# Performance work log

Measured on AMD Instinct MI355X. Metric: run time of the kernel, lower is better.

## Reference

```python
import jax, jax.numpy as jnp
import numpy as np

V = 32000; D = 1024; L = 2; H = 16; KVH = 4; HD = D // H; E = 8; FF = 2048; K = 2
B = 2; S = 1024; WINDOW = 4096; THETA = 10000.0; EPS = 1e-6


def setup_inputs() -> dict:
    key = jax.random.key(0)
    ks = jax.random.split(key, 12)
    std = 0.02
    return {
        'tokens': jax.random.randint(ks[0], (B, S), 0, V),
        'tok_emb': jax.random.normal(ks[1], (V, D), jnp.float32),  # nn.Embedding default N(0,1)
        'norm1_w': jnp.ones((L, D), jnp.float32),
        'norm2_w': jnp.ones((L, D), jnp.float32),
        'wq': jax.random.normal(ks[2], (L, D, D), jnp.float32) * std,
        'wk': jax.random.normal(ks[3], (L, KVH * HD, D), jnp.float32) * std,
        'wv': jax.random.normal(ks[4], (L, KVH * HD, D), jnp.float32) * std,
        'wo': jax.random.normal(ks[5], (L, D, D), jnp.float32) * std,
        'router_w': jax.random.normal(ks[6], (L, E, D), jnp.float32) * (std / np.sqrt(D)),
        'w1': jax.random.normal(ks[7], (L, E, FF, D), jnp.float32) * std,
        'w2': jax.random.normal(ks[8], (L, E, FF, D), jnp.float32) * std,
        'w3': jax.random.normal(ks[9], (L, E, D, FF), jnp.float32) * std,
        'normf_w': jnp.ones((D,), jnp.float32),
        'head_w': jax.random.normal(ks[10], (V, D), jnp.float32) * std,
    }


def rmsnorm(x, w):
    # F.normalize(x, dim=-1, eps) * w * sqrt(d)
    n = jnp.linalg.norm(x, axis=-1, keepdims=True)
    return x / jnp.maximum(n, EPS) * w * np.float32(np.sqrt(x.shape[-1]))


def rope(x, cos, sin):
    # x: (b, s, h, hd); pairs are interleaved (even, odd) per view_as_complex
    x2 = x.reshape(x.shape[:-1] + (-1, 2))
    x0, x1 = x2[..., 0], x2[..., 1]
    o0 = x0 * cos - x1 * sin
    o1 = x0 * sin + x1 * cos
    return jnp.stack([o0, o1], axis=-1).reshape(x.shape)


def attention(x, wq, wk, wv, wo, cos, sin):
    b, s, _ = x.shape
    q = (x @ wq.T).reshape(b, s, H, HD)
    k = (x @ wk.T).reshape(b, s, KVH, HD)
    v = (x @ wv.T).reshape(b, s, KVH, HD)
    q = rope(q, cos, sin)
    k = rope(k, cos, sin)
    g = H // KVH
    k = jnp.repeat(k, g, axis=2)
    v = jnp.repeat(v, g, axis=2)
    scores = jnp.einsum('bqhd,bkhd->bhqk', q, k) / np.float32(np.sqrt(HD))
    i = jnp.arange(s)[:, None]; j = jnp.arange(s)[None, :]
    allow = (j <= i) & (i - j < WINDOW)  # causal + sliding window
    scores = jnp.where(allow, scores, -jnp.inf)
    attn = jax.nn.softmax(scores, axis=-1)
    out = jnp.einsum('bhqk,bkhd->bqhd', attn, v).reshape(b, s, D)
    return out @ wo.T


def moe(x, router_w, w1, w2, w3):
    b, s, d = x.shape
    logits = jnp.einsum('bsd,ed->bse', x, router_w)
    probs = jax.nn.softmax(logits, axis=-1)
    _, idx = jax.lax.top_k(probs, K)                      # (b, s, K)
    mask = jax.nn.one_hot(idx, E, dtype=x.dtype).sum(-2)  # (b, s, E) binary
    xt = x.reshape(-1, d)           # (T, d)
    mt = mask.reshape(-1, E)        # (T, E)
    # Dense masked dispatch: every expert computed on all tokens, combine masks to zero
    u = jnp.einsum('td,efd->etf', xt, w1)
    g = jax.nn.silu(u) * jnp.einsum('td,efd->etf', xt, w2)
    y = jnp.einsum('etf,edf->etd', g, w3)
    out = jnp.einsum('etd,te->td', y, mt).reshape(b, s, d)  # unweighted combine (per source)
    # aux losses
    z_loss = jnp.mean(jax.scipy.special.logsumexp(logits, axis=-1)) ** 2
    load = probs.sum(axis=0)  # (s, E), matching probs.sum(dim=0) in source
    load_loss = (jnp.std(load, ddof=1) / jnp.mean(load)) ** 2
    aux = 0.001 * z_loss + 0.001 * load_loss
    return out, aux


def _rope_tables(dtype):
    freqs = 1.0 / (THETA ** (np.arange(0, HD, 2, dtype=np.float32) / HD))
    ang = np.arange(S, dtype=np.float32)[:, None] * freqs[None, :]
    cos = jnp.asarray(np.cos(ang), dtype)[None, :, None, :]
    sin = jnp.asarray(np.sin(ang), dtype)[None, :, None, :]
    return cos, sin


def reference(tokens, tok_emb, norm1_w, norm2_w, wq, wk, wv, wo, router_w, w1, w2, w3, normf_w, head_w):
    x = tok_emb[tokens]  # (B, S, D)
    cos, sin = _rope_tables(x.dtype)
    attn_scale = np.float32(1.0 / np.sqrt(2.0 * L))
    aux_total = jnp.zeros((), x.dtype)
    for l in range(L):
        x = x + attn_scale * attention(rmsnorm(x, norm1_w[l]), wq[l], wk[l], wv[l], wo[l], cos, sin)
        mo, aux = moe(rmsnorm(x, norm2_w[l]), router_w[l], w1[l], w2[l], w3[l])
        x = x + mo
        aux_total = aux_total + aux
    logits = rmsnorm(x, normf_w) @ head_w.T
    return logits, aux_total
```

## Files before the change

kernel.cpp:

```cpp
#include <hip/hip_runtime.h>
#include <math.h>

#define DEV __device__ __forceinline__

using v8s = __attribute__((ext_vector_type(8))) short;
using v4f = __attribute__((ext_vector_type(4))) float;

DEV short f2bf(float f) {
    unsigned u = __float_as_uint(f);
    unsigned r = (u + 0x7fffu + ((u >> 16) & 1u)) >> 16;
    return (short)(unsigned short)r;
}
DEV float bf2f(short s) {
    return __uint_as_float(((unsigned)(unsigned short)s) << 16);
}

DEV void gload16(const short* g, short* l) {
    __builtin_amdgcn_global_load_lds((const __attribute__((address_space(1))) void*)g,
                                     (__attribute__((address_space(3))) void*)l,
                                     16, 0, 0);
}

DEV void raw_barrier() { asm volatile("s_barrier" ::: "memory"); }

DEV float block_sum256(float v, float* red) {
    __syncthreads();
#pragma unroll
    for (int o = 32; o >= 1; o >>= 1) v += __shfl_down(v, o, 64);
    if ((threadIdx.x & 63) == 0) red[threadIdx.x >> 6] = v;
    __syncthreads();
    return red[0] + red[1] + red[2] + red[3];
}
DEV float block_max256(float v, float* red) {
    __syncthreads();
#pragma unroll
    for (int o = 32; o >= 1; o >>= 1) v = fmaxf(v, __shfl_down(v, o, 64));
    if ((threadIdx.x & 63) == 0) red[threadIdx.x >> 6] = v;
    __syncthreads();
    return fmaxf(fmaxf(red[0], red[1]), fmaxf(red[2], red[3]));
}


__global__ __launch_bounds__(256) void conv_tile(const float* __restrict__ src,
                                                 short* __restrict__ hi, short* __restrict__ lo,
                                                 long nGroups, int Kg, long chunkRows, long chunkPanelStride) {
    const long panelElems = 128L * Kg * 8;
    for (long idx = (long)blockIdx.x * 256 + threadIdx.x; idx < nGroups; idx += (long)gridDim.x * 256) {
        long rrow = idx / Kg; int g = (int)(idx - rrow * Kg);
        long c = rrow / chunkRows; int ri = (int)(rrow - c * chunkRows);
        long panel = c * chunkPanelStride + (ri >> 7);
        long dst = panel * panelElems + ((long)(g >> 2) << 12) + ((long)(g & 3) << 10) + ((long)(ri & 127) << 3);
        const float4 f0 = ((const float4*)src)[idx * 2];
        const float4 f1 = ((const float4*)src)[idx * 2 + 1];
        short h0 = f2bf(f0.x), h1 = f2bf(f0.y), h2 = f2bf(f0.z), h3 = f2bf(f0.w);
        short h4 = f2bf(f1.x), h5 = f2bf(f1.y), h6 = f2bf(f1.z), h7 = f2bf(f1.w);
        *(ushort4*)(hi + dst)     = make_ushort4((unsigned short)h0, (unsigned short)h1,
                                                 (unsigned short)h2, (unsigned short)h3);
        *(ushort4*)(hi + dst + 4) = make_ushort4((unsigned short)h4, (unsigned short)h5,
                                                 (unsigned short)h6, (unsigned short)h7);
        if (lo) {
            short l0 = f2bf(f0.x - bf2f(h0)), l1 = f2bf(f0.y - bf2f(h1));
            short l2 = f2bf(f0.z - bf2f(h2)), l3 = f2bf(f0.w - bf2f(h3));
            short l4 = f2bf(f1.x - bf2f(h4)), l5 = f2bf(f1.y - bf2f(h5));
            short l6 = f2bf(f1.z - bf2f(h6)), l7 = f2bf(f1.w - bf2f(h7));
            *(ushort4*)(lo + dst)     = make_ushort4((unsigned short)l0, (unsigned short)l1,
                                                     (unsigned short)l2, (unsigned short)l3);
            *(ushort4*)(lo + dst + 4) = make_ushort4((unsigned short)l4, (unsigned short)l5,
                                                     (unsigned short)l6, (unsigned short)l7);
        }
    }
}

struct GemmP {
    const short* Ah; const short* Al;
    const short* Bh; const short* Bl;
    float* C; short* Ch; short* Cl;
    const int* cnt; const int* ppd; const int* lrow;
    long aPanelsZ;
    long strideAz;
    long strideBz, strideCz;
    int M, N, K, lda, ldc;
    float alpha;
    int outMode;
    int gqaB;
    int grouped;
    int causalSkip;
    int ntiles, G, Gx;
};

template<bool SPLIT>
__global__ __launch_bounds__(256) void gemm_bt128(GemmP p) {
    const int lid = blockIdx.x;
    const int xcd = lid & 7, sI = lid >> 3;
    const int gx = sI % p.Gx;
    const int mt = sI / p.Gx;
    const int gi = xcd + 8 * gx;
    if (gi >= p.G) return;
    const int nt = gi % p.ntiles;
    const int z  = gi / p.ntiles;
    if (p.causalSkip && nt > mt) return;

    const int tid = threadIdx.x;
    int Mz = p.grouped ? p.cnt[z] : p.M;
    if (mt * 128 >= Mz) return;

    long bOff;
    if (p.gqaB) { int b = z >> 4, h = z & 15; bOff = (long)(b * 4 + (h >> 2)) * p.strideBz; }
    else bOff = (long)z * p.strideBz;

    extern __shared__ short s0[];
    const int BUF = SPLIT ? 16384 : 8192;

    const int lane = tid & 63, w = tid >> 6;
    const int lr = lane & 15, lg = lane >> 4;
    const int wr = w >> 1, wc = w & 1;

    v4f acc[4][4];
#pragma unroll
    for (int i = 0; i < 4; ++i)
#pragma unroll
        for (int j = 0; j < 4; ++j) { acc[i][j][0] = 0.f; acc[i][j][1] = 0.f; acc[i][j][2] = 0.f; acc[i][j][3] = 0.f; }

    const short* bks  = p.Bh + bOff + (long)nt * 128 * p.K + (long)w * 1024 + lane * 8;
    const short* bksL = SPLIT ? p.Bl + bOff + (long)nt * 128 * p.K + (long)w * 1024 + lane * 8 : nullptr;

    long aPanel = (p.grouped ? (long)(p.ppd[z] >> 7) : (long)z * p.aPanelsZ) + mt;
    const short* aks  = p.Ah + aPanel * 128L * p.K + (long)w * 1024 + lane * 8;
    const short* aksL = SPLIT ? p.Al + aPanel * 128L * p.K + (long)w * 1024 + lane * 8 : nullptr;

    const int nIter = p.K >> 5;
    const int wb = w * 1024;
    {
        gload16(aks,       s0 + wb);
        gload16(aks + 512, s0 + wb + 512);
        gload16(bks,       s0 + 4096 + wb);
        gload16(bks + 512, s0 + 4096 + wb + 512);
        if (SPLIT) {
            gload16(aksL,       s0 + 8192 + wb);
            gload16(aksL + 512, s0 + 8192 + wb + 512);
            gload16(bksL,       s0 + 12288 + wb);
            gload16(bksL + 512, s0 + 12288 + wb + 512);
        }
    }
    for (int i = 0; i < nIter; ++i) {
        const int cur = i & 1;
        if (i + 1 < nIter) {
            raw_barrier();
            const long kb = (long)(i + 1) * 4096;
            short* base = s0 + (cur ^ 1) * BUF;
            gload16(aks + kb,       base + wb);
            gload16(aks + kb + 512, base + wb + 512);
            gload16(bks + kb,       base + 4096 + wb);
            gload16(bks + kb + 512, base + 4096 + wb + 512);
            if (SPLIT) {
                gload16(aksL + kb,       base + 8192 + wb);
                gload16(aksL + kb + 512, base + 8192 + wb + 512);
                gload16(bksL + kb,       base + 12288 + wb);
                gload16(bksL + kb + 512, base + 12288 + wb + 512);
            }
            if constexpr (SPLIT) asm volatile("s_waitcnt vmcnt(8)" ::: "memory");
            else                 asm volatile("s_waitcnt vmcnt(4)" ::: "memory");
        } else {
            asm volatile("s_waitcnt vmcnt(0)" ::: "memory");
        }
        raw_barrier();
        const short* base = s0 + cur * BUF;
        const int abase = lg * 1024 + (wr * 64 + lr) * 8;
        const int bbase = 4096 + lg * 1024 + (wc * 64 + lr) * 8;
        v8s ah[4], bh[4];
#pragma unroll
        for (int q = 0; q < 4; ++q) {
            ah[q] = *(const v8s*)(base + abase + q * 128);
            bh[q] = *(const v8s*)(base + bbase + q * 128);
        }
        if constexpr (SPLIT) {
            v8s al[4], bl[4];
#pragma unroll
            for (int q = 0; q < 4; ++q) {
                al[q] = *(const v8s*)(base + 8192 + abase + q * 128);
                bl[q] = *(const v8s*)(base + 8192 + bbase + q * 128);
            }
#pragma unroll
            for (int mi = 0; mi < 4; ++mi)
#pragma unroll
                for (int nj = 0; nj < 4; ++nj) {
                    acc[mi][nj] = __builtin_amdgcn_mfma_f32_16x16x32_bf16(ah[mi], bh[nj], acc[mi][nj], 0, 0, 0);
                    acc[mi][nj] = __builtin_amdgcn_mfma_f32_16x16x32_bf16(al[mi], bh[nj], acc[mi][nj], 0, 0, 0);
                    acc[mi][nj] = __builtin_amdgcn_mfma_f32_16x16x32_bf16(ah[mi], bl[nj], acc[mi][nj], 0, 0, 0);
                }
        } else {
#pragma unroll
            for (int mi = 0; mi < 4; ++mi)
#pragma unroll
                for (int nj = 0; nj < 4; ++nj)
                    acc[mi][nj] = __builtin_amdgcn_mfma_f32_16x16x32_bf16(ah[mi], bh[nj], acc[mi][nj], 0, 0, 0);
        }
    }

#pragma unroll
    for (int mi = 0; mi < 4; ++mi) {
        const int mrow = mt * 128 + wr * 64 + mi * 16 + lg * 4;
#pragma unroll
        for (int nj = 0; nj < 4; ++nj) {
            const int ncol = nt * 128 + wc * 64 + nj * 16 + lr;
            if (ncol < p.N) {
#pragma unroll
                for (int rr = 0; rr < 4; ++rr) {
                    const int m = mrow + rr;
                    if (m < Mz) {
                        float v = acc[mi][nj][rr] * p.alpha;
                        long crow;
                        if (p.grouped == 1)      crow = p.ppd[z] + m;
                        else if (p.grouped == 2) crow = p.lrow[z * 2048 + m];
                        else                     crow = m;
                        long co = (long)z * p.strideCz + crow * (long)p.ldc + ncol;
                        if (p.outMode == 0) p.C[co] = v;
                        else                p.C[co] += v;
                    }
                }
            }
        }
    }
}

template<bool SPLIT>
__global__ __launch_bounds__(512) void gemm_bt256(GemmP p) {
    const int lid = blockIdx.x;
    const int xcd = lid & 7, sI = lid >> 3;
    const int gx = sI % p.Gx;
    const int mt = sI / p.Gx;
    const int gi = xcd + 8 * gx;
    if (gi >= p.G) return;
    const int nt = gi % p.ntiles;
    const int z  = gi / p.ntiles;
    if (p.causalSkip && nt > 2 * mt + 1) return;

    const int tid = threadIdx.x;
    int Mz = p.grouped ? p.cnt[z] : p.M;
    if (mt * 256 >= Mz) return;

    long bOff;
    if (p.gqaB) { int b = z >> 4, h = z & 15; bOff = (long)(b * 4 + (h >> 2)) * p.strideBz; }
    else bOff = (long)z * p.strideBz;

    extern __shared__ short s0[];
    const int BUF = SPLIT ? 24576 : 12288;

    const int lane = tid & 63, w = tid >> 6;
    const int lr = lane & 15, lg = lane >> 4;
    const int wr = w >> 1, wc = w & 1;

    v4f acc[4][4];
#pragma unroll
    for (int i = 0; i < 4; ++i)
#pragma unroll
        for (int j = 0; j < 4; ++j) { acc[i][j][0] = 0.f; acc[i][j][1] = 0.f; acc[i][j][2] = 0.f; acc[i][j][3] = 0.f; }

    const short* bks  = p.Bh + bOff + (long)nt * 128 * p.K + (long)w * 512 + lane * 8;
    const short* bksL = SPLIT ? p.Bl + bOff + (long)nt * 128 * p.K + (long)w * 512 + lane * 8 : nullptr;
    const long aPanelBase = (p.grouped ? (long)(p.ppd[z] >> 7) : (long)z * p.aPanelsZ) + 2L * mt;
    const int u0 = 2 * w, u1 = 2 * w + 1;
    const short* aks0  = p.Ah + (aPanelBase + (u0 >> 3)) * 128L * p.K + (long)(u0 & 7) * 512 + lane * 8;
    const short* aks1  = p.Ah + (aPanelBase + (u1 >> 3)) * 128L * p.K + (long)(u1 & 7) * 512 + lane * 8;
    const short* aks0L = SPLIT ? p.Al + (aPanelBase + (u0 >> 3)) * 128L * p.K + (long)(u0 & 7) * 512 + lane * 8 : nullptr;
    const short* aks1L = SPLIT ? p.Al + (aPanelBase + (u1 >> 3)) * 128L * p.K + (long)(u1 & 7) * 512 + lane * 8 : nullptr;
    short* dA0 = s0 + u0 * 512;
    short* dA1 = s0 + u1 * 512;
    short* dB  = s0 + 8192 + w * 512;

    const int nIter = p.K >> 5;
    {
        gload16(aks0, dA0);
        gload16(aks1, dA1);
        gload16(bks,  dB);
        if (SPLIT) {
            gload16(aks0L, dA0 + 12288);
            gload16(aks1L, dA1 + 12288);
            gload16(bksL,  dB + 12288);
        }
    }
    for (int i = 0; i < nIter; ++i) {
        const int cur = i & 1;
        if (i + 1 < nIter) {
            raw_barrier();
            const long kb = (long)(i + 1) * 4096;
            const int boff = (cur ^ 1) * BUF;
            gload16(aks0 + kb, dA0 + boff);
            gload16(aks1 + kb, dA1 + boff);
            gload16(bks + kb,  dB + boff);
            if (SPLIT) {
                gload16(aks0L + kb, dA0 + boff + 12288);
                gload16(aks1L + kb, dA1 + boff + 12288);
                gload16(bksL + kb,  dB + boff + 12288);
            }
            if constexpr (SPLIT) asm volatile("s_waitcnt vmcnt(6)" ::: "memory");
            else                 asm volatile("s_waitcnt vmcnt(3)" ::: "memory");
        } else {
            asm volatile("s_waitcnt vmcnt(0)" ::: "memory");
        }
        raw_barrier();
        const short* base = s0 + cur * BUF;
        const int abase = (wr >> 1) * 4096 + lg * 1024 + ((wr & 1) * 64 + lr) * 8;
        const int bbase = 8192 + lg * 1024 + (wc * 64 + lr) * 8;
        v8s ah[4], bh[4];
#pragma unroll
        for (int q = 0; q < 4; ++q) {
            ah[q] = *(const v8s*)(base + abase + q * 128);
            bh[q] = *(const v8s*)(base + bbase + q * 128);
        }
        if constexpr (SPLIT) {
            v8s al[4], bl[4];
#pragma unroll
            for (int q = 0; q < 4; ++q) {
                al[q] = *(const v8s*)(base + 12288 + abase + q * 128);
                bl[q] = *(const v8s*)(base + 12288 + bbase + q * 128);
            }
#pragma unroll
            for (int mi = 0; mi < 4; ++mi)
#pragma unroll
                for (int nj = 0; nj < 4; ++nj) {
                    acc[mi][nj] = __builtin_amdgcn_mfma_f32_16x16x32_bf16(ah[mi], bh[nj], acc[mi][nj], 0, 0, 0);
                    acc[mi][nj] = __builtin_amdgcn_mfma_f32_16x16x32_bf16(al[mi], bh[nj], acc[mi][nj], 0, 0, 0);
                    acc[mi][nj] = __builtin_amdgcn_mfma_f32_16x16x32_bf16(ah[mi], bl[nj], acc[mi][nj], 0, 0, 0);
                }
        } else {
#pragma unroll
            for (int mi = 0; mi < 4; ++mi)
#pragma unroll
                for (int nj = 0; nj < 4; ++nj)
                    acc[mi][nj] = __builtin_amdgcn_mfma_f32_16x16x32_bf16(ah[mi], bh[nj], acc[mi][nj], 0, 0, 0);
        }
    }

#pragma unroll
    for (int mi = 0; mi < 4; ++mi) {
        const int mrow = mt * 256 + wr * 64 + mi * 16 + lg * 4;
#pragma unroll
        for (int nj = 0; nj < 4; ++nj) {
            const int ncol = nt * 128 + wc * 64 + nj * 16 + lr;
            if (ncol < p.N) {
#pragma unroll
                for (int rr = 0; rr < 4; ++rr) {
                    const int m = mrow + rr;
                    if (m < Mz) {
                        float v = acc[mi][nj][rr] * p.alpha;
                        long crow;
                        if (p.grouped == 1)      crow = p.ppd[z] + m;
                        else if (p.grouped == 2) crow = p.lrow[z * 2048 + m];
                        else                     crow = m;
                        long co = (long)z * p.strideCz + crow * (long)p.ldc + ncol;
                        if (p.outMode == 0) p.C[co] = v;
                        else                p.C[co] += v;
                    }
                }
            }
        }
    }
}

__global__ __launch_bounds__(256) void gemm_pv(GemmP p) {
    const int lid = blockIdx.x;
    const int xcd = lid & 7, sI = lid >> 3;
    const int gx = sI % 4;
    const int mt = sI / 4;
    const int z = xcd + 8 * gx;
    const int tid = threadIdx.x;

    const int b = z >> 4, h = z & 15;
    const long bOff = (long)(b * 4 + (h >> 2)) * p.strideBz;

    extern __shared__ short s0[];
    short* Ahs = s0;
    short* Bhs = s0 + 4096;
    short* Als = s0 + 8192;
    short* Bls = s0 + 12288;

    const int lane = tid & 63, w = tid >> 6;
    const int lr = lane & 15, lg = lane >> 4;
    const int wr = w >> 1, wc = w & 1;

    v4f acc[4][4];
#pragma unroll
    for (int i = 0; i < 4; ++i)
#pragma unroll
        for (int j = 0; j < 4; ++j) { acc[i][j][0] = 0.f; acc[i][j][1] = 0.f; acc[i][j][2] = 0.f; acc[i][j][3] = 0.f; }

    const short* bks  = p.Bh + bOff + (long)w * 1024 + lane * 8;
    const short* bksL = p.Bl + bOff + (long)w * 1024 + lane * 8;

    const int r = tid & 127;
    const int kgA = tid >> 7;
    const int am = mt * 128 + r;
    const long arowoff = (long)z * p.strideAz + (long)am * p.lda;
    const short* aH = p.Ah + arowoff + kgA * 16;
    const short* aL = p.Al + arowoff + kgA * 16;
    short* sA0 = s0 + (kgA * 256 + r) * 8; short* sA1 = sA0 + 1024;
    short* sA0l = s0 + 8192 + (kgA * 256 + r) * 8; short* sA1l = sA0l + 1024;

    const int kEnd = min(p.K, (mt + 1) * 128);
    const int wb = w * 1024;
    for (int k0 = 0; k0 < kEnd; k0 += 32) {
        const long kb = (long)k0 * 128;
        uint4 a0 = *(const uint4*)(aH + k0);
        uint4 a1 = *(const uint4*)(aH + k0 + 8);
        uint4 a0l = *(const uint4*)(aL + k0);
        uint4 a1l = *(const uint4*)(aL + k0 + 8);
        __syncthreads();
        gload16(bks + kb,       Bhs + wb);
        gload16(bks + kb + 512, Bhs + wb + 512);
        gload16(bksL + kb,       Bls + wb);
        gload16(bksL + kb + 512, Bls + wb + 512);
        *(uint4*)sA0 = a0; *(uint4*)sA1 = a1;
        *(uint4*)sA0l = a0l; *(uint4*)sA1l = a1l;
        __syncthreads();
        const int abase = lg * 1024 + (wr * 64 + lr) * 8;
        const int bbase = lg * 1024 + (wc * 64 + lr) * 8;
        v8s ah[4], bh[4], al[4], bl[4];
#pragma unroll
        for (int q = 0; q < 4; ++q) {
            ah[q] = *(const v8s*)(Ahs + abase + q * 128);
            bh[q] = *(const v8s*)(Bhs + bbase + q * 128);
            al[q] = *(const v8s*)(Als + abase + q * 128);
            bl[q] = *(const v8s*)(Bls + bbase + q * 128);
        }
#pragma unroll
        for (int mi = 0; mi < 4; ++mi)
#pragma unroll
            for (int nj = 0; nj < 4; ++nj) {
                acc[mi][nj] = __builtin_amdgcn_mfma_f32_16x16x32_bf16(ah[mi], bh[nj], acc[mi][nj], 0, 0, 0);
                acc[mi][nj] = __builtin_amdgcn_mfma_f32_16x16x32_bf16(al[mi], bh[nj], acc[mi][nj], 0, 0, 0);
                acc[mi][nj] = __builtin_amdgcn_mfma_f32_16x16x32_bf16(ah[mi], bl[nj], acc[mi][nj], 0, 0, 0);
            }
    }

#pragma unroll
    for (int mi = 0; mi < 4; ++mi) {
        const int mrow = mt * 128 + wr * 64 + mi * 16 + lg * 4;
#pragma unroll
        for (int nj = 0; nj < 4; ++nj) {
            const int ncol = wc * 64 + nj * 16 + lr;
            if (ncol < 64) {
#pragma unroll
                for (int rr = 0; rr < 4; ++rr) {
                    const int m = mrow + rr;
                    float v = acc[mi][nj][rr];
                    int grow = b * 1024 + m, col = h * 64 + ncol;
                    long dst = ((long)(grow >> 7)) * 131072 + ((long)(col >> 5) << 12)
                             + ((long)((col >> 3) & 3) << 10) + ((long)(grow & 127) << 3) + (col & 7);
                    short hi = f2bf(v);
                    p.Ch[dst] = hi;
                    p.Cl[dst] = f2bf(v - bf2f(hi));
                }
            }
        }
    }
}

__global__ __launch_bounds__(256) void embed_kernel(const int* toks, const float* emb, float* X) {
    const int t = blockIdx.x;
    const int tok = toks[t];
    const float4* s = (const float4*)(emb + (size_t)tok * 1024);
    float4* d = (float4*)(X + (size_t)t * 1024);
    d[threadIdx.x] = s[threadIdx.x];
}

__global__ __launch_bounds__(256) void rmsnorm_split(const float* X, const float* w, short* oh, short* ol) {
    __shared__ float red[4];
    const long t = blockIdx.x;
    const float* r = X + t * 1024;
    float ss = 0.f;
    for (int j = threadIdx.x; j < 1024; j += 256) { float f = r[j]; ss += f * f; }
    ss = block_sum256(ss, red);
    const float sc = 32.f / fmaxf(sqrtf(ss), 1e-6f);
    if (threadIdx.x < 128) {
        const int g = threadIdx.x, f = g * 8;
        float v[8];
#pragma unroll
        for (int j = 0; j < 8; ++j) v[j] = r[f + j] * sc * w[f + j];
        long dst = (t >> 7) * 131072 + ((long)(g >> 2) << 12) + ((long)(g & 3) << 10) + ((t & 127) << 3);
        short h[8], lo[8];
#pragma unroll
        for (int j = 0; j < 8; ++j) { h[j] = f2bf(v[j]); lo[j] = f2bf(v[j] - bf2f(h[j])); }
        *(ushort4*)(oh + dst)     = make_ushort4((unsigned short)h[0], (unsigned short)h[1], (unsigned short)h[2], (unsigned short)h[3]);
        *(ushort4*)(oh + dst + 4) = make_ushort4((unsigned short)h[4], (unsigned short)h[5], (unsigned short)h[6], (unsigned short)h[7]);
        *(ushort4*)(ol + dst)     = make_ushort4((unsigned short)lo[0], (unsigned short)lo[1], (unsigned short)lo[2], (unsigned short)lo[3]);
        *(ushort4*)(ol + dst + 4) = make_ushort4((unsigned short)lo[4], (unsigned short)lo[5], (unsigned short)lo[6], (unsigned short)lo[7]);
    }
}

struct RopeF { float f[32]; };

__global__ __launch_bounds__(256) void rope_fused_kernel(const float* QKV,
                                                         short* QH, short* QL,
                                                         short* KH, short* KL,
                                                         short* VH, short* VL, RopeF rf) {
    const int bid = blockIdx.x;
    if (bid < 4096) {
        const int idx = bid * 256 + threadIdx.x;
        const int pp = idx & 31, h = (idx >> 5) & 15, s = (idx >> 9) & 1023, b = idx >> 19;
        const float* src = QKV + ((size_t)(b * 1024 + s)) * 1536 + h * 64 + 2 * pp;
        const float x0 = src[0], x1 = src[1];
        const float ang = (float)s * rf.f[pp];
        float sn, cs; sincosf(ang, &sn, &cs);
        const float o0 = x0 * cs - x1 * sn, o1 = x0 * sn + x1 * cs;
        const int z = b * 16 + h, d = 2 * pp;
        const long off = (long)z * 65536 + (long)(s >> 7) * 8192
                       + ((long)(d >> 5) << 12) + ((long)((d >> 3) & 3) << 10)
                       + ((long)(s & 127) << 3) + (d & 7);
        short h0 = f2bf(o0); QH[off] = h0; QL[off] = f2bf(o0 - bf2f(h0));
        short h1 = f2bf(o1); QH[off + 1] = h1; QL[off + 1] = f2bf(o1 - bf2f(h1));
    } else if (bid < 5120) {
        const int idx = (bid - 4096) * 256 + threadIdx.x;
        const int pp = idx & 31, kv = (idx >> 5) & 3, s = (idx >> 7) & 1023, b = idx >> 17;
        const float* src = QKV + ((size_t)(b * 1024 + s)) * 1536 + 1024 + kv * 64 + 2 * pp;
        const float x0 = src[0], x1 = src[1];
        const float ang = (float)s * rf.f[pp];
        float sn, cs; sincosf(ang, &sn, &cs);
        const float o0 = x0 * cs - x1 * sn, o1 = x0 * sn + x1 * cs;
        const int z = b * 4 + kv, d = 2 * pp;
        const long off = (long)z * 65536 + (long)(s >> 7) * 8192
                       + ((long)(d >> 5) << 12) + ((long)((d >> 3) & 3) << 10)
                       + ((long)(s & 127) << 3) + (d & 7);
        short h0 = f2bf(o0); KH[off] = h0; KL[off] = f2bf(o0 - bf2f(h0));
        short h1 = f2bf(o1); KH[off + 1] = h1; KL[off + 1] = f2bf(o1 - bf2f(h1));
    } else {
        const int idx = (bid - 5120) * 256 + threadIdx.x;
        const int d = idx & 63, kv = (idx >> 6) & 3, s = (idx >> 8) & 1023, b = idx >> 18;
        const float f = QKV[((size_t)(b * 1024 + s)) * 1536 + 1280 + kv * 64 + d];
        const int z = b * 4 + kv;
        const long off = (long)z * 131072 + ((long)(s >> 5) << 12) + ((long)((s >> 3) & 3) << 10)
                       + ((long)d << 3) + (s & 7);
        short hi = f2bf(f);
        VH[off] = hi; VL[off] = f2bf(f - bf2f(hi));
        VH[off + 512] = 0; VL[off + 512] = 0;
    }
}

__global__ __launch_bounds__(256) void attn_softmax(float* SC) {
    const long row = blockIdx.x;
    const int i = (int)(row & 1023);
    float* r = SC + row * 1024;
    __shared__ float buf[1024];
    __shared__ float red[4];
    const int n = i + 1;
    for (int j = threadIdx.x; j < n; j += 256) buf[j] = r[j];
    __syncthreads();
    float m = -INFINITY;
    for (int j = threadIdx.x; j < n; j += 256) m = fmaxf(m, buf[j]);
    m = block_max256(m, red);
    float s = 0.f;
    for (int j = threadIdx.x; j < n; j += 256) { float e = expf(buf[j] - m); buf[j] = e; s += e; }
    s = block_sum256(s, red);
    const float inv = 1.f / s;
    short* rh = (short*)r;
    short* rl = rh + 1024;
    __syncthreads();
    for (int j = threadIdx.x; j < 1024; j += 256) {
        float pv = (j < n) ? buf[j] * inv : 0.f;
        short hi = f2bf(pv);
        rh[j] = hi;
        rl[j] = f2bf(pv - bf2f(hi));
    }
}

__global__ __launch_bounds__(256) void router_kernel(const float* X, const float* wn, const float* rw,
                                                     float* probs, float* lse, int* cnt, int* ltok, int* lrow) {
    __shared__ float xs[1024];
    __shared__ float red[4];
    __shared__ float lg[8];
    const int t = blockIdx.x;
    const float* r = X + (size_t)t * 1024;
    for (int j = threadIdx.x; j < 1024; j += 256) xs[j] = r[j];
    __syncthreads();
    float ss = 0.f;
    for (int j = threadIdx.x; j < 1024; j += 256) ss += xs[j] * xs[j];
    ss = block_sum256(ss, red);
    const float sc = 32.f / fmaxf(sqrtf(ss), 1e-6f);
    float acc[8] = {0, 0, 0, 0, 0, 0, 0, 0};
    for (int j = threadIdx.x; j < 1024; j += 256) {
        const float xv = xs[j] * wn[j];
#pragma unroll
        for (int e = 0; e < 8; ++e) acc[e] += xv * rw[e * 1024 + j];
    }
#pragma unroll
    for (int e = 0; e < 8; ++e) {
        float s = block_sum256(acc[e], red);
        if (threadIdx.x == 0) lg[e] = s * sc;
    }
    __syncthreads();
    if (threadIdx.x == 0) {
        float m = lg[0];
        for (int e = 1; e < 8; ++e) m = fmaxf(m, lg[e]);
        float ex[8], se = 0.f;
        for (int e = 0; e < 8; ++e) { ex[e] = expf(lg[e] - m); se += ex[e]; }
        const float inv = 1.f / se;
        float pr[8];
        for (int e = 0; e < 8; ++e) { pr[e] = ex[e] * inv; probs[(size_t)t * 8 + e] = pr[e]; }
        lse[t] = m + logf(se);
        int i1 = 0;
        for (int e = 1; e < 8; ++e) if (pr[e] > pr[i1]) i1 = e;
        int i2 = (i1 == 0) ? 1 : 0;
        for (int e = 0; e < 8; ++e) if (e != i1 && pr[e] > pr[i2]) i2 = e;
        int s1 = atomicAdd(&cnt[i1], 1); ltok[i1 * 2048 + s1] = t; lrow[i1 * 2048 + s1] = 2 * t;
        int s2 = atomicAdd(&cnt[i2], 1); ltok[i2 * 2048 + s2] = t; lrow[i2 * 2048 + s2] = 2 * t + 1;
    }
}

__global__ void prefix_kernel(const int* cnt, int* ppd) {
    if (threadIdx.x == 0 && blockIdx.x == 0) {
        int a = 0;
        for (int e = 0; e < 8; ++e) { ppd[e] = a; a += ((cnt[e] + 255) >> 8) << 8; }
    }
}

__global__ __launch_bounds__(256) void gather_kernel(const short* XNH, const short* XNL,
                                                     const int* cnt, const int* ppd, const int* ltok,
                                                     short* GXNH, short* GXNL) {
    const int e = blockIdx.y, i = blockIdx.x;
    if (i >= cnt[e]) return;
    const int t = ltok[e * 2048 + i];
    const int pd = ppd[e] + i;
    const int plane = threadIdx.x >> 7, g = threadIdx.x & 127;
    const long goff = ((long)(g >> 2) << 12) + ((long)(g & 3) << 10);
    const long src = (long)(t >> 7) * 131072 + goff + ((t & 127) << 3);
    const long dst = (long)(pd >> 7) * 131072 + goff + ((pd & 127) << 3);
    const short* S = plane ? XNL : XNH;
    short* D = plane ? GXNL : GXNH;
    *(uint4*)(D + dst) = *(const uint4*)(S + src);
}

__global__ __launch_bounds__(256) void silu_mul(const float* U, short* HH, short* HL) {
    const int row = blockIdx.x, g = threadIdx.x;
    const float* ur = U + (long)row * 4096 + g * 8;
    const float4 u0 = *(const float4*)ur, u1 = *(const float4*)(ur + 4);
    const float4 g0 = *(const float4*)(ur + 2048), g1 = *(const float4*)(ur + 2052);
    float h[8];
    h[0] = (u0.x / (1.f + expf(-u0.x))) * g0.x;
    h[1] = (u0.y / (1.f + expf(-u0.y))) * g0.y;
    h[2] = (u0.z / (1.f + expf(-u0.z))) * g0.z;
    h[3] = (u0.w / (1.f + expf(-u0.w))) * g0.w;
    h[4] = (u1.x / (1.f + expf(-u1.x))) * g1.x;
    h[5] = (u1.y / (1.f + expf(-u1.y))) * g1.y;
    h[6] = (u1.z / (1.f + expf(-u1.z))) * g1.z;
    h[7] = (u1.w / (1.f + expf(-u1.w))) * g1.w;
    const long dst = (long)(row >> 7) * 262144 + ((long)(g >> 2) << 12) + ((long)(g & 3) << 10) + ((row & 127) << 3);
    short hh[8], ll[8];
#pragma unroll
    for (int j = 0; j < 8; ++j) { hh[j] = f2bf(h[j]); ll[j] = f2bf(h[j] - bf2f(hh[j])); }
    *(ushort4*)(HH + dst)     = make_ushort4((unsigned short)hh[0], (unsigned short)hh[1], (unsigned short)hh[2], (unsigned short)hh[3]);
    *(ushort4*)(HH + dst + 4) = make_ushort4((unsigned short)hh[4], (unsigned short)hh[5], (unsigned short)hh[6], (unsigned short)hh[7]);
    *(ushort4*)(HL + dst)     = make_ushort4((unsigned short)ll[0], (unsigned short)ll[1], (unsigned short)ll[2], (unsigned short)ll[3]);
    *(ushort4*)(HL + dst + 4) = make_ushort4((unsigned short)ll[4], (unsigned short)ll[5], (unsigned short)ll[6], (unsigned short)ll[7]);
}

__global__ __launch_bounds__(256) void combine_kernel(float* X, const float* Y) {
    const int i4 = blockIdx.x * 256 + threadIdx.x;
    const int t = i4 >> 8, d4 = i4 & 255;
    float4 x = ((float4*)X)[i4];
    const float4 a = ((const float4*)Y)[(size_t)(2 * t) * 256 + d4];
    const float4 b = ((const float4*)Y)[(size_t)(2 * t + 1) * 256 + d4];
    x.x += a.x + b.x; x.y += a.y + b.y; x.z += a.z + b.z; x.w += a.w + b.w;
    ((float4*)X)[i4] = x;
}

__global__ __launch_bounds__(256) void aux_kernel(const float* probs, const float* lse, float* auxb, int layer) {
    __shared__ float red[4];
    float sl = 0.f;
    for (int t = threadIdx.x; t < 2048; t += 256) sl += lse[t];
    sl = block_sum256(sl, red);
    float s1 = 0.f, s2 = 0.f;
    for (int i = threadIdx.x; i < 8192; i += 256) {
        const float l = probs[i] + probs[8192 + i];
        s1 += l; s2 += l * l;
    }
    s1 = block_sum256(s1, red);
    s2 = block_sum256(s2, red);
    if (threadIdx.x == 0) {
        const float ml = sl / 2048.f;
        const float mean = s1 / 8192.f;
        const float var = fmaxf((s2 - s1 * s1 / 8192.f) / 8191.f, 0.f);
        auxb[layer] = 0.001f * (ml * ml + var / (mean * mean));
    }
}

__global__ void finalize_aux(const float* auxb, float* out) {
    if (threadIdx.x == 0 && blockIdx.x == 0)
        out[(size_t)2 * 1024 * 32000] = auxb[0] + auxb[1];
}

static void run_gemm128(hipStream_t s, bool split, GemmP& p, int ntiles, int mtiles, int zdim) {
    p.ntiles = ntiles;
    p.G = ntiles * zdim;
    p.Gx = (p.G + 7) >> 3;
    long nb = 8L * p.Gx * mtiles;
    dim3 g((unsigned)nb, 1, 1), b(256);
    if (split) gemm_bt128<true><<<g, b, 65536, s>>>(p);
    else       gemm_bt128<false><<<g, b, 32768, s>>>(p);
}

static void run_gemm256(hipStream_t s, bool split, GemmP& p, int ntiles, int mtiles, int zdim) {
    p.ntiles = ntiles;
    p.G = ntiles * zdim;
    p.Gx = (p.G + 7) >> 3;
    long nb = 8L * p.Gx * mtiles;
    dim3 g((unsigned)nb, 1, 1), b(512);
    if (split) gemm_bt256<true><<<g, b, 98304, s>>>(p);
    else       gemm_bt256<false><<<g, b, 49152, s>>>(p);
}

static void run_tile(hipStream_t s, const float* src, short* hi, short* lo,
                     long rows, int K, long chunkRows, long chunkPanelStride) {
    long groups = rows * (K / 8);
    long nb = (groups + 255) / 256; if (nb > 2048) nb = 2048;
    conv_tile<<<(unsigned)nb, 256, 0, s>>>(src, hi, lo, groups, K / 8, chunkRows, chunkPanelStride);
}

extern "C" void kernel_launch(void* const* d_in, const int* in_sizes, int n_in,
                              void* d_out, int out_size, void* d_ws, size_t ws_size,
                              hipStream_t stream) {
    (void)in_sizes; (void)n_in; (void)out_size; (void)ws_size;
    const int*   tokens = (const int*)d_in[0];
    const float* tok_emb = (const float*)d_in[1];
    const float* norm1 = (const float*)d_in[2];
    const float* norm2 = (const float*)d_in[3];
    const float* wq = (const float*)d_in[4];
    const float* wk = (const float*)d_in[5];
    const float* wv = (const float*)d_in[6];
    const float* wo = (const float*)d_in[7];
    const float* rw = (const float*)d_in[8];
    const float* w1 = (const float*)d_in[9];
    const float* w2 = (const float*)d_in[10];
    const float* w3 = (const float*)d_in[11];
    const float* normf = (const float*)d_in[12];
    const float* headw = (const float*)d_in[13];
    float* out = (float*)d_out;

    char* w = (char*)d_ws;
    const size_t MB = 1024ull * 1024ull;
    float* X    = (float*)(w + 0);
    short* XNH  = (short*)(w + 8 * MB);
    short* XNL  = (short*)(w + 12 * MB);
    short* QRH  = (short*)(w + 16 * MB);
    short* QRL  = (short*)(w + 20 * MB);
    short* AOH  = QRH;
    short* AOL  = QRL;
    short* KRH  = (short*)(w + 24 * MB);
    short* KRL  = (short*)(w + 25 * MB);
    short* VTH  = (short*)(w + 26 * MB);
    short* VTL  = (short*)(w + 28 * MB);
    float* QKV  = (float*)(w + 32 * MB);
    float* SC   = (float*)(w + 32 * MB);
    short* GXNH = (short*)(w + 32 * MB);
    short* GXNL = (short*)(w + 44 * MB);
    float* U    = (float*)(w + 56 * MB);
    short* HH   = (short*)(w + 152 * MB);
    short* HL   = (short*)(w + 176 * MB);
    float* Y    = (float*)(w + 200 * MB);
    float* PROBS= (float*)(w + 216 * MB);
    float* LSE  = (float*)(w + 216 * MB + 65536);
    int*   CNT  = (int*)  (w + 216 * MB + 73728);
    int*   PPD  = (int*)  (w + 216 * MB + 73856);
    int*   LTOK = (int*)  (w + 216 * MB + 74240);
    int*   LROW = (int*)  (w + 216 * MB + 74240 + 65536);
    float* AUXB = (float*)(w + 216 * MB + 74240 + 131072);
    short* WQKVH = (short*)(w + 218 * MB);
    short* WQKVL = (short*)(w + 224 * MB);
    short* WOH   = (short*)(w + 230 * MB);
    short* WOL   = (short*)(w + 234 * MB);
    short* W12H  = (short*)(w + 238 * MB);
    short* W12L  = (short*)(w + 302 * MB);
    short* W3H   = (short*)(w + 366 * MB);
    short* W3L   = (short*)(w + 398 * MB);
    short* HDH   = (short*)(w + 302 * MB);

    RopeF rf;
    for (int i = 0; i < 32; ++i) {
        float t = (float)pow(10000.0, (double)(2 * i) / 64.0);
        rf.f[i] = 1.0f / t;
    }

    for (int l = 0; l < 2; ++l) {
        long qo = (long)l * 1572864;
        run_tile(stream, wq + (long)l * 1048576, WQKVH + qo,           WQKVL + qo,           1024, 1024, 1024, 8);
        run_tile(stream, wk + (long)l * 262144,  WQKVH + qo + 1048576, WQKVL + qo + 1048576, 256, 1024, 256, 2);
        run_tile(stream, wv + (long)l * 262144,  WQKVH + qo + 1310720, WQKVL + qo + 1310720, 256, 1024, 256, 2);
    }
    run_tile(stream, wo, WOH, WOL, 2048, 1024, 2048, 16);

    embed_kernel<<<2048, 256, 0, stream>>>(tokens, tok_emb, X);

    for (int l = 0; l < 2; ++l) {
        const bool msp = (l == 0);
        run_tile(stream, w1 + (long)l * 16777216, W12H,           msp ? W12L : nullptr,           16384, 1024, 2048, 32);
        run_tile(stream, w2 + (long)l * 16777216, W12H + 2097152, msp ? W12L + 2097152 : nullptr, 16384, 1024, 2048, 32);
        run_tile(stream, w3 + (long)l * 16777216, W3H,            msp ? W3L : nullptr,            8192, 2048, 8192, 64);

        rmsnorm_split<<<2048, 256, 0, stream>>>(X, norm1 + l * 1024, XNH, XNL);

        { GemmP p = {}; p.Ah = XNH; p.Al = XNL; p.Bh = WQKVH + (long)l * 1572864; p.Bl = WQKVL + (long)l * 1572864;
          p.C = QKV; p.M = 2048; p.N = 1536; p.K = 1024; p.aPanelsZ = 16; p.ldc = 1536; p.alpha = 1.f;
          run_gemm128(stream, true, p, 12, 16, 1); }

        rope_fused_kernel<<<7168, 256, 0, stream>>>(QKV, QRH, QRL, KRH, KRL, VTH, VTL, rf);

        { GemmP p = {}; p.Ah = QRH; p.Al = QRL; p.Bh = KRH; p.Bl = KRL; p.C = SC;
          p.M = 1024; p.N = 1024; p.K = 64; p.aPanelsZ = 8; p.ldc = 1024;
          p.strideBz = 65536; p.strideCz = 1048576;
          p.alpha = 0.125f; p.gqaB = 1; p.causalSkip = 1;
          run_gemm256(stream, true, p, 8, 4, 32); }

        attn_softmax<<<32768, 256, 0, stream>>>(SC);

        { GemmP p = {}; p.Ah = (short*)SC; p.Al = (short*)SC + 1024; p.Bh = VTH; p.Bl = VTL; p.Ch = AOH; p.Cl = AOL;
          p.M = 1024; p.N = 64; p.K = 1024; p.lda = 2048;
          p.strideAz = 2097152; p.strideBz = 131072;
          gemm_pv<<<dim3(256), dim3(256), 32768, stream>>>(p); }

        { GemmP p = {}; p.Ah = AOH; p.Al = AOL; p.Bh = WOH + (long)l * 1048576; p.Bl = WOL + (long)l * 1048576; p.C = X;
          p.M = 2048; p.N = 1024; p.K = 1024; p.aPanelsZ = 16; p.ldc = 1024;
          p.alpha = 0.5f; p.outMode = 1;
          run_gemm128(stream, true, p, 8, 16, 1); }

        rmsnorm_split<<<2048, 256, 0, stream>>>(X, norm2 + l * 1024, XNH, XNL);
        hipMemsetAsync(CNT, 0, 8 * sizeof(int), stream);
        router_kernel<<<2048, 256, 0, stream>>>(X, norm2 + l * 1024, rw + (size_t)l * 8 * 1024,
                                                PROBS, LSE, CNT, LTOK, LROW);
        prefix_kernel<<<1, 64, 0, stream>>>(CNT, PPD);
        { dim3 gg(2048, 8); gather_kernel<<<gg, 256, 0, stream>>>(XNH, XNL, CNT, PPD, LTOK, GXNH, GXNL); }

        if (msp) {
            GemmP p = {}; p.Ah = GXNH; p.Al = GXNL; p.Bh = W12H; p.Bl = W12L; p.C = U;
            p.M = 2048; p.N = 4096; p.K = 1024; p.ldc = 4096;
            p.strideBz = 4194304; p.strideCz = 0; p.alpha = 1.f; p.grouped = 1;
            p.cnt = CNT; p.ppd = PPD; p.lrow = LROW;
            run_gemm128(stream, true, p, 32, 16, 8);
        } else {
            GemmP p = {}; p.Ah = GXNH; p.Al = GXNL; p.Bh = W12H; p.Bl = W12L; p.C = U;
            p.M = 2048; p.N = 4096; p.K = 1024; p.ldc = 4096;
            p.strideBz = 4194304; p.strideCz = 0; p.alpha = 1.f; p.grouped = 1;
            p.cnt = CNT; p.ppd = PPD; p.lrow = LROW;
            run_gemm256(stream, false, p, 32, 8, 8);
        }
        silu_mul<<<6144, 256, 0, stream>>>(U, HH, HL);
        if (msp) {
            GemmP p = {}; p.Ah = HH; p.Al = HL; p.Bh = W3H; p.Bl = W3L; p.C = Y;
            p.M = 2048; p.N = 1024; p.K = 2048; p.ldc = 1024;
            p.strideBz = 2097152; p.strideCz = 0; p.alpha = 1.f; p.grouped = 2;
            p.cnt = CNT; p.ppd = PPD; p.lrow = LROW;
            run_gemm128(stream, true, p, 8, 16, 8);
        } else {
            GemmP p = {}; p.Ah = HH; p.Al = HL; p.Bh = W3H; p.Bl = W3L; p.C = Y;
            p.M = 2048; p.N = 1024; p.K = 2048; p.ldc = 1024;
            p.strideBz = 2097152; p.strideCz = 0; p.alpha = 1.f; p.grouped = 2;
            p.cnt = CNT; p.ppd = PPD; p.lrow = LROW;
            run_gemm256(stream, false, p, 8, 8, 8);
        }
        combine_kernel<<<2048, 256, 0, stream>>>(X, Y);
        aux_kernel<<<1, 256, 0, stream>>>(PROBS, LSE, AUXB, l);

        if (l == 0)
            run_tile(stream, headw, HDH, nullptr, 32000, 1024, 32000, 250);
    }

    rmsnorm_split<<<2048, 256, 0, stream>>>(X, normf, XNH, XNL);
    { GemmP p = {}; p.Ah = XNH; p.Bh = HDH; p.C = out;
      p.M = 2048; p.N = 32000; p.K = 1024; p.aPanelsZ = 16; p.ldc = 32000; p.alpha = 1.f;
      run_gemm256(stream, false, p, 250, 8, 1); }
    finalize_aux<<<1, 1, 0, stream>>>(AUXB, out);
}
```

Before: 2.020 ms.

## Triple-buffer gemm_bt256 K pipeline and group M tiles for L2 reuse

The 256-row GEMM now keeps three LDS buffers and prefetches two K-steps ahead, waiting with deeper vmcnt thresholds, so global loads have more time to complete before MFMA use. Both GEMM kernels also remap block indices so that consecutive blocks on an XCD walk an inner group of M tiles before moving along N, which aims to raise L2 reuse of B panels. The cost is more LDS per block (up to 144 KB in split mode), which can lower occupancy, plus extra integer index math.

```diff
diff --git a/kernel.cpp b/kernel.cpp
--- a/kernel.cpp
+++ b/kernel.cpp
@@ -86,14 +86,17 @@
     int grouped;
     int causalSkip;
     int ntiles, G, Gx;
+    int mtIn;
 };
 
 template<bool SPLIT>
 __global__ __launch_bounds__(256) void gemm_bt128(GemmP p) {
     const int lid = blockIdx.x;
     const int xcd = lid & 7, sI = lid >> 3;
-    const int gx = sI % p.Gx;
-    const int mt = sI / p.Gx;
+    const int mtLo = sI % p.mtIn;
+    const int t1 = sI / p.mtIn;
+    const int gx = t1 % p.Gx;
+    const int mt = (t1 / p.Gx) * p.mtIn + mtLo;
     const int gi = xcd + 8 * gx;
     if (gi >= p.G) return;
     const int nt = gi % p.ntiles;
@@ -227,8 +230,10 @@
 __global__ __launch_bounds__(512) void gemm_bt256(GemmP p) {
     const int lid = blockIdx.x;
     const int xcd = lid & 7, sI = lid >> 3;
-    const int gx = sI % p.Gx;
-    const int mt = sI / p.Gx;
+    const int mtLo = sI % p.mtIn;
+    const int t1 = sI / p.mtIn;
+    const int gx = t1 % p.Gx;
+    const int mt = (t1 / p.Gx) * p.mtIn + mtLo;
     const int gi = xcd + 8 * gx;
     if (gi >= p.G) return;
     const int nt = gi % p.ntiles;
@@ -264,35 +269,30 @@
     const short* aks1  = p.Ah + (aPanelBase + (u1 >> 3)) * 128L * p.K + (long)(u1 & 7) * 512 + lane * 8;
     const short* aks0L = SPLIT ? p.Al + (aPanelBase + (u0 >> 3)) * 128L * p.K + (long)(u0 & 7) * 512 + lane * 8 : nullptr;
     const short* aks1L = SPLIT ? p.Al + (aPanelBase + (u1 >> 3)) * 128L * p.K + (long)(u1 & 7) * 512 + lane * 8 : nullptr;
-    short* dA0 = s0 + u0 * 512;
-    short* dA1 = s0 + u1 * 512;
-    short* dB  = s0 + 8192 + w * 512;
+    const int oA0 = u0 * 512, oA1 = u1 * 512, oB = 8192 + w * 512;
 
     const int nIter = p.K >> 5;
-    {
-        gload16(aks0, dA0);
-        gload16(aks1, dA1);
-        gload16(bks,  dB);
+    auto stage = [&](int it, short* base) {
+        const long kb = (long)it * 4096;
+        gload16(aks0 + kb, base + oA0);
+        gload16(aks1 + kb, base + oA1);
+        gload16(bks + kb,  base + oB);
         if (SPLIT) {
-            gload16(aks0L, dA0 + 12288);
-            gload16(aks1L, dA1 + 12288);
-            gload16(bksL,  dB + 12288);
-        }
-    }
+            gload16(aks0L + kb, base + oA0 + 12288);
+            gload16(aks1L + kb, base + oA1 + 12288);
+            gload16(bksL + kb,  base + oB + 12288);
+        }
+    };
+    stage(0, s0);
+    if (nIter > 1) stage(1, s0 + BUF);
+    int cur = 0, nxt = 2;
     for (int i = 0; i < nIter; ++i) {
-        const int cur = i & 1;
-        if (i + 1 < nIter) {
-            raw_barrier();
-            const long kb = (long)(i + 1) * 4096;
-            const int boff = (cur ^ 1) * BUF;
-            gload16(aks0 + kb, dA0 + boff);
-            gload16(aks1 + kb, dA1 + boff);
-            gload16(bks + kb,  dB + boff);
-            if (SPLIT) {
-                gload16(aks0L + kb, dA0 + boff + 12288);
-                gload16(aks1L + kb, dA1 + boff + 12288);
-                gload16(bksL + kb,  dB + boff + 12288);
-            }
+        raw_barrier();
+        if (i + 2 < nIter) {
+            stage(i + 2, s0 + nxt * BUF);
+            if constexpr (SPLIT) asm volatile("s_waitcnt vmcnt(12)" ::: "memory");
+            else                 asm volatile("s_waitcnt vmcnt(6)" ::: "memory");
+        } else if (i + 1 < nIter) {
             if constexpr (SPLIT) asm volatile("s_waitcnt vmcnt(6)" ::: "memory");
             else                 asm volatile("s_waitcnt vmcnt(3)" ::: "memory");
         } else {
@@ -330,6 +330,8 @@
                 for (int nj = 0; nj < 4; ++nj)
                     acc[mi][nj] = __builtin_amdgcn_mfma_f32_16x16x32_bf16(ah[mi], bh[nj], acc[mi][nj], 0, 0, 0);
         }
+        cur = (cur == 2) ? 0 : cur + 1;
+        nxt = (nxt == 2) ? 0 : nxt + 1;
     }
 
 #pragma unroll
@@ -688,24 +690,26 @@
         out[(size_t)2 * 1024 * 32000] = auxb[0] + auxb[1];
 }
 
-static void run_gemm128(hipStream_t s, bool split, GemmP& p, int ntiles, int mtiles, int zdim) {
+static void run_gemm128(hipStream_t s, bool split, GemmP& p, int ntiles, int mtiles, int zdim, int mtIn) {
     p.ntiles = ntiles;
     p.G = ntiles * zdim;
     p.Gx = (p.G + 7) >> 3;
+    p.mtIn = mtIn;
     long nb = 8L * p.Gx * mtiles;
     dim3 g((unsigned)nb, 1, 1), b(256);
     if (split) gemm_bt128<true><<<g, b, 65536, s>>>(p);
     else       gemm_bt128<false><<<g, b, 32768, s>>>(p);
 }
 
-static void run_gemm256(hipStream_t s, bool split, GemmP& p, int ntiles, int mtiles, int zdim) {
+static void run_gemm256(hipStream_t s, bool split, GemmP& p, int ntiles, int mtiles, int zdim, int mtIn) {
     p.ntiles = ntiles;
     p.G = ntiles * zdim;
     p.Gx = (p.G + 7) >> 3;
+    p.mtIn = mtIn;
     long nb = 8L * p.Gx * mtiles;
     dim3 g((unsigned)nb, 1, 1), b(512);
-    if (split) gemm_bt256<true><<<g, b, 98304, s>>>(p);
-    else       gemm_bt256<false><<<g, b, 49152, s>>>(p);
+    if (split) gemm_bt256<true><<<g, b, 147456, s>>>(p);
+    else       gemm_bt256<false><<<g, b, 73728, s>>>(p);
 }
 
 static void run_tile(hipStream_t s, const float* src, short* hi, short* lo,
@@ -799,7 +803,7 @@
 
         { GemmP p = {}; p.Ah = XNH; p.Al = XNL; p.Bh = WQKVH + (long)l * 1572864; p.Bl = WQKVL + (long)l * 1572864;
           p.C = QKV; p.M = 2048; p.N = 1536; p.K = 1024; p.aPanelsZ = 16; p.ldc = 1536; p.alpha = 1.f;
-          run_gemm128(stream, true, p, 12, 16, 1); }
+          run_gemm128(stream, true, p, 12, 16, 1, 4); }
 
         rope_fused_kernel<<<7168, 256, 0, stream>>>(QKV, QRH, QRL, KRH, KRL, VTH, VTL, rf);
 
@@ -807,7 +811,7 @@
           p.M = 1024; p.N = 1024; p.K = 64; p.aPanelsZ = 8; p.ldc = 1024;
           p.strideBz = 65536; p.strideCz = 1048576;
           p.alpha = 0.125f; p.gqaB = 1; p.causalSkip = 1;
-          run_gemm256(stream, true, p, 8, 4, 32); }
+          run_gemm256(stream, true, p, 8, 4, 32, 1); }
 
         attn_softmax<<<32768, 256, 0, stream>>>(SC);
 
@@ -819,7 +823,7 @@
         { GemmP p = {}; p.Ah = AOH; p.Al = AOL; p.Bh = WOH + (long)l * 1048576; p.Bl = WOL + (long)l * 1048576; p.C = X;
           p.M = 2048; p.N = 1024; p.K = 1024; p.aPanelsZ = 16; p.ldc = 1024;
           p.alpha = 0.5f; p.outMode = 1;
-          run_gemm128(stream, true, p, 8, 16, 1); }
+          run_gemm128(stream, true, p, 8, 16, 1, 4); }
 
         rmsnorm_split<<<2048, 256, 0, stream>>>(X, norm2 + l * 1024, XNH, XNL);
         hipMemsetAsync(CNT, 0, 8 * sizeof(int), stream);
@@ -833,13 +837,13 @@
             p.M = 2048; p.N = 4096; p.K = 1024; p.ldc = 4096;
             p.strideBz = 4194304; p.strideCz = 0; p.alpha = 1.f; p.grouped = 1;
             p.cnt = CNT; p.ppd = PPD; p.lrow = LROW;
-            run_gemm128(stream, true, p, 32, 16, 8);
+            run_gemm128(stream, true, p, 32, 16, 8, 4);
         } else {
             GemmP p = {}; p.Ah = GXNH; p.Al = GXNL; p.Bh = W12H; p.Bl = W12L; p.C = U;
             p.M = 2048; p.N = 4096; p.K = 1024; p.ldc = 4096;
             p.strideBz = 4194304; p.strideCz = 0; p.alpha = 1.f; p.grouped = 1;
             p.cnt = CNT; p.ppd = PPD; p.lrow = LROW;
-            run_gemm256(stream, false, p, 32, 8, 8);
+            run_gemm256(stream, false, p, 32, 8, 8, 2);
         }
         silu_mul<<<6144, 256, 0, stream>>>(U, HH, HL);
         if (msp) {
@@ -847,13 +851,13 @@
             p.M = 2048; p.N = 1024; p.K = 2048; p.ldc = 1024;
             p.strideBz = 2097152; p.strideCz = 0; p.alpha = 1.f; p.grouped = 2;
             p.cnt = CNT; p.ppd = PPD; p.lrow = LROW;
-            run_gemm128(stream, true, p, 8, 16, 8);
+            run_gemm128(stream, true, p, 8, 16, 8, 4);
         } else {
             GemmP p = {}; p.Ah = HH; p.Al = HL; p.Bh = W3H; p.Bl = W3L; p.C = Y;
             p.M = 2048; p.N = 1024; p.K = 2048; p.ldc = 1024;
             p.strideBz = 2097152; p.strideCz = 0; p.alpha = 1.f; p.grouped = 2;
             p.cnt = CNT; p.ppd = PPD; p.lrow = LROW;
-            run_gemm256(stream, false, p, 8, 8, 8);
+            run_gemm256(stream, false, p, 8, 8, 8, 2);
         }
         combine_kernel<<<2048, 256, 0, stream>>>(X, Y);
         aux_kernel<<<1, 256, 0, stream>>>(PROBS, LSE, AUXB, l);
@@ -865,6 +869,6 @@
     rmsnorm_split<<<2048, 256, 0, stream>>>(X, normf, XNH, XNL);
     { GemmP p = {}; p.Ah = XNH; p.Bh = HDH; p.C = out;
       p.M = 2048; p.N = 32000; p.K = 1024; p.aPanelsZ = 16; p.ldc = 32000; p.alpha = 1.f;
-      run_gemm256(stream, false, p, 250, 8, 1); }
+      run_gemm256(stream, false, p, 250, 8, 1, 4); }
     finalize_aux<<<1, 1, 0, stream>>>(AUXB, out);
 }
```

Result: no change. 2.058 ms (+1.9%).
